# Performance work log

Hardware: AMD Instinct MI355X
Metric: run time of the kernel (lower is better)

## Reference

```python
import jax, jax.numpy as jnp
import numpy as np

D_MODEL = 4096
D_FIBER = 16
D_CONTROL = 64
EMA_MOMENTUM = 0.9


def setup_inputs() -> dict:
    key = jax.random.key(0)
    k_h, k_f, k_w1, k_w2 = jax.random.split(key, 4)
    B, S = 4, 2048
    hidden = jax.random.normal(k_h, (B, S, D_MODEL), dtype=jnp.float32)
    # torch nn.Linear stores weight as [out, in]; fiber_proj init: normal std=0.02
    W_fiber = jax.random.normal(k_f, (D_FIBER, D_MODEL), dtype=jnp.float32) * 0.02
    # predictor[0]: Linear(d_model+d_fiber, d_control) with default torch init (uniform)
    fan_in1 = D_MODEL + D_FIBER
    bound1 = 1.0 / np.sqrt(fan_in1)
    W1 = jax.random.uniform(k_w1, (D_CONTROL, fan_in1), dtype=jnp.float32, minval=-bound1, maxval=bound1)
    b1 = jnp.zeros((D_CONTROL,), dtype=jnp.float32)
    # predictor[-2]: Linear(d_control, 1), weight normal std=0.01, bias zero
    W2 = jax.random.normal(k_w2, (1, D_CONTROL), dtype=jnp.float32) * 0.01
    b2 = jnp.zeros((1,), dtype=jnp.float32)
    lam = jnp.asarray(1.0, dtype=jnp.float32)
    return {"hidden": hidden, "W_fiber": W_fiber, "W1": W1, "b1": b1, "W2": W2, "b2": b2, "lam": lam}


def _causal_ema(delta_h, alpha):
    # h_t = alpha*h_{t-1} + (1-alpha)*d_t, h_{-1} = 0. delta_h: [B,S]
    B = delta_h.shape[0]
    def step(h_prev, d_t):
        h_t = alpha * h_prev + (1.0 - alpha) * d_t
        return h_t, h_t
    _, hs = jax.lax.scan(step, jnp.zeros((B,), delta_h.dtype), jnp.swapaxes(delta_h, 0, 1))
    return jnp.swapaxes(hs, 0, 1)  # [B,S]


def reference(hidden, W_fiber, W1, b1, W2, b2, lam):
    h = hidden.astype(jnp.float32)                      # [B,S,D]
    fiber = jnp.einsum('bsd,fd->bsf', h, W_fiber)       # [B,S,16]
    combined = jnp.concatenate([h, fiber], axis=-1)     # [B,S,D+16]
    z = jax.nn.gelu(jnp.einsum('bsc,kc->bsk', combined, W1) + b1, approximate=False)
    delta_h = jax.nn.softplus(jnp.einsum('bsk,ok->bso', z, W2) + b2)[..., 0]  # [B,S]
    field = _causal_ema(delta_h, EMA_MOMENTUM)          # [B,S]
    gate = jax.nn.sigmoid(-lam * field)
    return gate.astype(hidden.dtype), field.astype(hidden.dtype), delta_h.mean()
```

## Files before the change

kernel.cpp:

```cpp
#include <hip/hip_runtime.h>
#include <hip/hip_bf16.h>

#define D_MODEL 4096
#define NTOK    8192
#define SEQ     2048

typedef short bf16x8 __attribute__((ext_vector_type(8)));
typedef float f32x4  __attribute__((ext_vector_type(4)));

__device__ __forceinline__ short f2bf(float x) {
  __hip_bfloat16 h = __float2bfloat16(x);
  return *reinterpret_cast<short*>(&h);
}
__device__ __forceinline__ float bfs2f(unsigned short u) {
  unsigned int x = ((unsigned int)u) << 16;
  float f;
  __builtin_memcpy(&f, &x, 4);
  return f;
}
__device__ __forceinline__ float bf2f(const void* p, size_t i) {
  return bfs2f(((const unsigned short*)p)[i]);
}

__device__ __forceinline__ void gload_lds16(const void* g, void* l) {
  __builtin_amdgcn_global_load_lds(
      (__attribute__((address_space(1))) void*)(g),
      (__attribute__((address_space(3))) void*)(l), 16, 0, 0);
}

__device__ __forceinline__ int sniff_wave(const unsigned short* p, int n) {
  int lane = threadIdx.x & 63;
  int S = n / 2 < 64 ? n / 2 : 64;
  bool act = lane < S;
  unsigned short ve = 0, vo = 0;
  if (act) { ve = p[2 * lane]; vo = p[2 * lane + 1]; }
  int ee = (ve >> 7) & 0xFF, eo = (vo >> 7) & 0xFF;
  bool ve_band   = (ve == 0) || (ve == 0x8000) || (ee >= 96 && ee <= 141);
  bool vo_bandnz = (vo != 0) && (vo != 0x8000) && (eo >= 96 && eo <= 141);
  int zp = __popcll(__ballot(act && ve == 0 && vo == 0));
  int ob = __popcll(__ballot(act && ve == 0 && vo_bandnz));
  int eb = __popcll(__ballot(act && ve_band));
  if (zp == S) return 1;
  if (4 * ob >= 3 * S) return 0;
  if (4 * eb >= 3 * S) return 1;
  return 0;
}

__device__ __forceinline__ float decode_lam(const void* lamp) {
  unsigned short l0 = *(const unsigned short*)lamp;
  int le = (l0 >> 7) & 0xFF;
  if (l0 != 0 && l0 != 0x8000 && le >= 96 && le <= 141)
    return bfs2f(l0);
  return *(const float*)lamp;
}
__device__ __forceinline__ float decode_b2(const void* p) {
  unsigned short c0 = *(const unsigned short*)p;
  int ce = (c0 >> 7) & 0xFF;
  if (c0 == 0) return 0.0f;
  if (c0 != 0x8000 && ce >= 96 && ce <= 141)
    return bfs2f(c0);
  return *(const float*)p;
}

__global__ __launch_bounds__(256) void fold_w1(const void* __restrict__ W1v,
                                               const void* __restrict__ Wfv,
                                               short* __restrict__ W1eff) {
  int n = blockIdx.x;
  int fw1 = sniff_wave((const unsigned short*)W1v, 64 * 4112);
  int fwf = sniff_wave((const unsigned short*)Wfv, 16 * D_MODEL);
  __shared__ float w1b[16];
  if (threadIdx.x < 16) {
    size_t idx = (size_t)n * 4112 + 4096 + threadIdx.x;
    w1b[threadIdx.x] = fw1 ? bf2f(W1v, idx) : ((const float*)W1v)[idx];
  }
  __syncthreads();
  for (int it = 0; it < 4; ++it) {
    int k0 = it * 1024 + threadIdx.x * 4;
    size_t idx = (size_t)n * 4112 + k0;
    float v0, v1, v2, v3;
    if (fw1) {
      ushort4 u = *(const ushort4*)((const unsigned short*)W1v + idx);
      v0 = bfs2f(u.x); v1 = bfs2f(u.y); v2 = bfs2f(u.z); v3 = bfs2f(u.w);
    } else {
      float4 f = *(const float4*)((const float*)W1v + idx);
      v0 = f.x; v1 = f.y; v2 = f.z; v3 = f.w;
    }
#pragma unroll
    for (int f = 0; f < 16; ++f) {
      size_t wi = (size_t)f * D_MODEL + k0;
      float w0, w1_, w2_, w3_;
      if (fwf) {
        ushort4 u = *(const ushort4*)((const unsigned short*)Wfv + wi);
        w0 = bfs2f(u.x); w1_ = bfs2f(u.y); w2_ = bfs2f(u.z); w3_ = bfs2f(u.w);
      } else {
        float4 fv = *(const float4*)((const float*)Wfv + wi);
        w0 = fv.x; w1_ = fv.y; w2_ = fv.z; w3_ = fv.w;
      }
      float s = w1b[f];
      v0 += s * w0; v1 += s * w1_; v2 += s * w2_; v3 += s * w3_;
    }
    ushort4 o;
    o.x = (unsigned short)f2bf(v0); o.y = (unsigned short)f2bf(v1);
    o.z = (unsigned short)f2bf(v2); o.w = (unsigned short)f2bf(v3);
    *(ushort4*)(W1eff + (size_t)n * D_MODEL + k0) = o;
  }
}

__global__ __launch_bounds__(64, 4) void gemm_part(const void* __restrict__ hid,
                                                   const short* __restrict__ B_,
                                                   float* __restrict__ part) {
  int t = blockIdx.x >> 3;
  int c = blockIdx.x & 7;
  int lane = threadIdx.x & 63;
  int m = lane & 15, kg = lane >> 4;

  __shared__ short As[16 * 512];

  int fhid = sniff_wave((const unsigned short*)hid, NTOK * D_MODEL);

  f32x4 acc0 = {0.f, 0.f, 0.f, 0.f};
  f32x4 acc1 = acc0, acc2 = acc0, acc3 = acc0;

  const short* Bp = B_ + (size_t)m * D_MODEL + c * 512 + kg * 8;

  if (fhid) {
#pragma unroll
    for (int n = 0; n < 16; ++n) {
      const char* src = (const char*)hid +
          ((size_t)(t * 16 + n) * D_MODEL + c * 512) * 2 +
          ((lane ^ (n & 7)) * 16);
      gload_lds16(src, (char*)As + n * 1024);
    }
    asm volatile("s_waitcnt vmcnt(0)" ::: "memory");
#pragma unroll
    for (int s = 0; s < 16; ++s) {
      int u = s * 4 + kg;
      bf16x8 a = *(const bf16x8*)((const char*)As + m * 1024 +
                                  ((u ^ (m & 7)) * 16));
      bf16x8 b0 = *(const bf16x8*)(Bp + (size_t)0 * 16 * D_MODEL + s * 32);
      bf16x8 b1 = *(const bf16x8*)(Bp + (size_t)1 * 16 * D_MODEL + s * 32);
      bf16x8 b2 = *(const bf16x8*)(Bp + (size_t)2 * 16 * D_MODEL + s * 32);
      bf16x8 b3 = *(const bf16x8*)(Bp + (size_t)3 * 16 * D_MODEL + s * 32);
      acc0 = __builtin_amdgcn_mfma_f32_16x16x32_bf16(a, b0, acc0, 0, 0, 0);
      acc1 = __builtin_amdgcn_mfma_f32_16x16x32_bf16(a, b1, acc1, 0, 0, 0);
      acc2 = __builtin_amdgcn_mfma_f32_16x16x32_bf16(a, b2, acc2, 0, 0, 0);
      acc3 = __builtin_amdgcn_mfma_f32_16x16x32_bf16(a, b3, acc3, 0, 0, 0);
    }
  } else {
    const float* Ap = (const float*)hid +
        (size_t)(t * 16 + m) * D_MODEL + c * 512 + kg * 8;
    for (int s = 0; s < 16; ++s) {
      float4 lo = *(const float4*)(Ap + s * 32);
      float4 hi = *(const float4*)(Ap + s * 32 + 4);
      bf16x8 a;
      a[0] = f2bf(lo.x); a[1] = f2bf(lo.y); a[2] = f2bf(lo.z); a[3] = f2bf(lo.w);
      a[4] = f2bf(hi.x); a[5] = f2bf(hi.y); a[6] = f2bf(hi.z); a[7] = f2bf(hi.w);
      bf16x8 b0 = *(const bf16x8*)(Bp + (size_t)0 * 16 * D_MODEL + s * 32);
      bf16x8 b1 = *(const bf16x8*)(Bp + (size_t)1 * 16 * D_MODEL + s * 32);
      bf16x8 b2 = *(const bf16x8*)(Bp + (size_t)2 * 16 * D_MODEL + s * 32);
      bf16x8 b3 = *(const bf16x8*)(Bp + (size_t)3 * 16 * D_MODEL + s * 32);
      acc0 = __builtin_amdgcn_mfma_f32_16x16x32_bf16(a, b0, acc0, 0, 0, 0);
      acc1 = __builtin_amdgcn_mfma_f32_16x16x32_bf16(a, b1, acc1, 0, 0, 0);
      acc2 = __builtin_amdgcn_mfma_f32_16x16x32_bf16(a, b2, acc2, 0, 0, 0);
      acc3 = __builtin_amdgcn_mfma_f32_16x16x32_bf16(a, b3, acc3, 0, 0, 0);
    }
  }

  float* po = part + ((size_t)c * NTOK + (size_t)t * 16) * 64;
#pragma unroll
  for (int r = 0; r < 4; ++r) {
    int row = kg * 4 + r;
    po[row * 64 + (m +  0)] = acc0[r];
    po[row * 64 + (m + 16)] = acc1[r];
    po[row * 64 + (m + 32)] = acc2[r];
    po[row * 64 + (m + 48)] = acc3[r];
  }
}

__global__ __launch_bounds__(256) void delta_ep(const float* __restrict__ part,
                                                const void* __restrict__ b1,
                                                const void* __restrict__ w2,
                                                const void* __restrict__ b2p,
                                                float* __restrict__ delta) {
  int tok = blockIdx.x * 16 + (threadIdx.x >> 4);
  int cid = threadIdx.x & 15;
  int fb1 = sniff_wave((const unsigned short*)b1, 64);
  int fw2 = sniff_wave((const unsigned short*)w2, 64);
  float y = 0.f;
#pragma unroll
  for (int j = 0; j < 4; ++j) {
    int col = cid + 16 * j;
    float s = 0.f;
#pragma unroll
    for (int c = 0; c < 8; ++c)
      s += part[((size_t)c * NTOK + tok) * 64 + col];
    s += fb1 ? bf2f(b1, col) : ((const float*)b1)[col];
    float g = 0.5f * s * (1.0f + erff(s * 0.70710678118654752f));
    y += g * (fw2 ? bf2f(w2, col) : ((const float*)w2)[col]);
  }
#pragma unroll
  for (int off = 1; off <= 8; off <<= 1) y += __shfl_xor(y, off, 64);
  if (cid == 0) {
    float x = y + decode_b2(b2p);
    float d = (x > 20.0f) ? x : log1pf(expf(x));
    delta[tok] = d;
  }
}

__global__ __launch_bounds__(256) void ema_out(const float* __restrict__ delta,
                                               const void* __restrict__ lamp,
                                               float* __restrict__ out) {
  int b    = threadIdx.x >> 6;
  int lane = threadIdx.x & 63;
  const float alpha = 0.9f;
  float d[32];
  const float* dp = delta + b * SEQ + lane * 32;
  float beta = 0.f, lsum = 0.f;
#pragma unroll
  for (int i = 0; i < 32; ++i) {
    d[i] = dp[i];
    lsum += d[i];
    beta = alpha * beta + 0.1f * d[i];
  }
  float accA = 0.03433683820292512f;
  float accB = beta;
  for (int off = 1; off < 64; off <<= 1) {
    float uA = __shfl_up(accA, off, 64);
    float uB = __shfl_up(accB, off, 64);
    if (lane >= off) {
      accB = accB + accA * uB;
      accA = accA * uA;
    }
  }
  float prev = __shfl_up(accB, 1, 64);
  float h = (lane == 0) ? 0.f : prev;
  float lam = decode_lam(lamp);
#pragma unroll
  for (int i = 0; i < 32; ++i) {
    h = alpha * h + 0.1f * d[i];
    float gate = 1.0f / (1.0f + expf(lam * h));
    out[b * SEQ + lane * 32 + i]        = gate;
    out[NTOK + b * SEQ + lane * 32 + i] = h;
  }
#pragma unroll
  for (int off = 32; off >= 1; off >>= 1) lsum += __shfl_xor(lsum, off, 64);
  __shared__ float bs[4];
  if (lane == 0) bs[b] = lsum;
  __syncthreads();
  if (threadIdx.x == 0)
    out[2 * NTOK] = (bs[0] + bs[1] + bs[2] + bs[3]) * (1.0f / 8192.0f);
}

extern "C" void kernel_launch(void* const* d_in, const int* in_sizes, int n_in,
                              void* d_out, int out_size, void* d_ws, size_t ws_size,
                              hipStream_t stream) {
  const void* hidden = d_in[0];
  const void* Wf     = d_in[1];
  const void* W1     = d_in[2];
  const void* b1     = d_in[3];
  const void* W2     = d_in[4];
  const void* b2     = d_in[5];
  const void* lam    = d_in[6];
  float* out = (float*)d_out;

  char* ws = (char*)d_ws;
  short* W1eff = (short*)ws;
  float* delta = (float*)(ws + (size_t)64 * D_MODEL * 2);
  float* part  = (float*)(ws + (size_t)64 * D_MODEL * 2 + NTOK * 4);

  fold_w1<<<64, 256, 0, stream>>>(W1, Wf, W1eff);
  gemm_part<<<4096, 64, 0, stream>>>(hidden, W1eff, part);
  delta_ep<<<512, 256, 0, stream>>>(part, b1, W2, b2, delta);
  ema_out<<<1, 256, 0, stream>>>(delta, lam, out);
}
```

Before: 232.9 us.

## Split gemm_part output columns across four waves per block

Each gemm block now runs 256 threads (four waves), and each wave computes one 16-column slice of the 64 outputs instead of one wave computing all four. The shared A tile load is split across the waves and followed by a block barrier. The aim is more waves in flight to hide latency in this memory-bound GEMM, at the cost of a __syncthreads per block and each wave re-reading the shared A tile from LDS.

```diff
diff --git a/kernel.cpp b/kernel.cpp
--- a/kernel.cpp
+++ b/kernel.cpp
@@ -106,11 +106,12 @@
   }
 }
 
-__global__ __launch_bounds__(64, 4) void gemm_part(const void* __restrict__ hid,
-                                                   const short* __restrict__ B_,
-                                                   float* __restrict__ part) {
+__global__ __launch_bounds__(256, 6) void gemm_part(const void* __restrict__ hid,
+                                                    const short* __restrict__ B_,
+                                                    float* __restrict__ part) {
   int t = blockIdx.x >> 3;
   int c = blockIdx.x & 7;
+  int w    = threadIdx.x >> 6;
   int lane = threadIdx.x & 63;
   int m = lane & 15, kg = lane >> 4;
 
@@ -118,33 +119,26 @@
 
   int fhid = sniff_wave((const unsigned short*)hid, NTOK * D_MODEL);
 
-  f32x4 acc0 = {0.f, 0.f, 0.f, 0.f};
-  f32x4 acc1 = acc0, acc2 = acc0, acc3 = acc0;
-
-  const short* Bp = B_ + (size_t)m * D_MODEL + c * 512 + kg * 8;
+  f32x4 acc = {0.f, 0.f, 0.f, 0.f};
+  const short* Bp = B_ + (size_t)(w * 16 + m) * D_MODEL + c * 512 + kg * 8;
 
   if (fhid) {
 #pragma unroll
-    for (int n = 0; n < 16; ++n) {
+    for (int i = 0; i < 4; ++i) {
+      int n = w * 4 + i;
       const char* src = (const char*)hid +
           ((size_t)(t * 16 + n) * D_MODEL + c * 512) * 2 +
           ((lane ^ (n & 7)) * 16);
       gload_lds16(src, (char*)As + n * 1024);
     }
-    asm volatile("s_waitcnt vmcnt(0)" ::: "memory");
+    __syncthreads();
 #pragma unroll
     for (int s = 0; s < 16; ++s) {
       int u = s * 4 + kg;
       bf16x8 a = *(const bf16x8*)((const char*)As + m * 1024 +
                                   ((u ^ (m & 7)) * 16));
-      bf16x8 b0 = *(const bf16x8*)(Bp + (size_t)0 * 16 * D_MODEL + s * 32);
-      bf16x8 b1 = *(const bf16x8*)(Bp + (size_t)1 * 16 * D_MODEL + s * 32);
-      bf16x8 b2 = *(const bf16x8*)(Bp + (size_t)2 * 16 * D_MODEL + s * 32);
-      bf16x8 b3 = *(const bf16x8*)(Bp + (size_t)3 * 16 * D_MODEL + s * 32);
-      acc0 = __builtin_amdgcn_mfma_f32_16x16x32_bf16(a, b0, acc0, 0, 0, 0);
-      acc1 = __builtin_amdgcn_mfma_f32_16x16x32_bf16(a, b1, acc1, 0, 0, 0);
-      acc2 = __builtin_amdgcn_mfma_f32_16x16x32_bf16(a, b2, acc2, 0, 0, 0);
-      acc3 = __builtin_amdgcn_mfma_f32_16x16x32_bf16(a, b3, acc3, 0, 0, 0);
+      bf16x8 b = *(const bf16x8*)(Bp + s * 32);
+      acc = __builtin_amdgcn_mfma_f32_16x16x32_bf16(a, b, acc, 0, 0, 0);
     }
   } else {
     const float* Ap = (const float*)hid +
@@ -155,14 +149,8 @@
       bf16x8 a;
       a[0] = f2bf(lo.x); a[1] = f2bf(lo.y); a[2] = f2bf(lo.z); a[3] = f2bf(lo.w);
       a[4] = f2bf(hi.x); a[5] = f2bf(hi.y); a[6] = f2bf(hi.z); a[7] = f2bf(hi.w);
-      bf16x8 b0 = *(const bf16x8*)(Bp + (size_t)0 * 16 * D_MODEL + s * 32);
-      bf16x8 b1 = *(const bf16x8*)(Bp + (size_t)1 * 16 * D_MODEL + s * 32);
-      bf16x8 b2 = *(const bf16x8*)(Bp + (size_t)2 * 16 * D_MODEL + s * 32);
-      bf16x8 b3 = *(const bf16x8*)(Bp + (size_t)3 * 16 * D_MODEL + s * 32);
-      acc0 = __builtin_amdgcn_mfma_f32_16x16x32_bf16(a, b0, acc0, 0, 0, 0);
-      acc1 = __builtin_amdgcn_mfma_f32_16x16x32_bf16(a, b1, acc1, 0, 0, 0);
-      acc2 = __builtin_amdgcn_mfma_f32_16x16x32_bf16(a, b2, acc2, 0, 0, 0);
-      acc3 = __builtin_amdgcn_mfma_f32_16x16x32_bf16(a, b3, acc3, 0, 0, 0);
+      bf16x8 b = *(const bf16x8*)(Bp + s * 32);
+      acc = __builtin_amdgcn_mfma_f32_16x16x32_bf16(a, b, acc, 0, 0, 0);
     }
   }
 
@@ -170,10 +158,7 @@
 #pragma unroll
   for (int r = 0; r < 4; ++r) {
     int row = kg * 4 + r;
-    po[row * 64 + (m +  0)] = acc0[r];
-    po[row * 64 + (m + 16)] = acc1[r];
-    po[row * 64 + (m + 32)] = acc2[r];
-    po[row * 64 + (m + 48)] = acc3[r];
+    po[row * 64 + w * 16 + m] = acc[r];
   }
 }
 
@@ -269,7 +254,7 @@
   float* part  = (float*)(ws + (size_t)64 * D_MODEL * 2 + NTOK * 4);
 
   fold_w1<<<64, 256, 0, stream>>>(W1, Wf, W1eff);
-  gemm_part<<<4096, 64, 0, stream>>>(hidden, W1eff, part);
+  gemm_part<<<4096, 256, 0, stream>>>(hidden, W1eff, part);
   delta_ep<<<512, 256, 0, stream>>>(part, b1, W2, b2, delta);
   ema_out<<<1, 256, 0, stream>>>(delta, lam, out);
 }
```

Measured after the change: 262.4 us. 1.13x slower.
